# Kernel tuning notes

Hardware: AMD Instinct MI355X
Metric: run time of the kernel (lower is better)

## Reference

```python
import jax, jax.numpy as jnp
import numpy as np

T, N, D, H = 1024, 8, 1024, 16
DK = D // H
NEG_INF = jnp.finfo(jnp.float32).min


def setup_inputs() -> dict:
    key = jax.random.key(0)
    ks = jax.random.split(key, 4)
    x = jax.random.normal(ks[0], (T, N, D), dtype=jnp.float32)
    # xavier-uniform-like scale for in_proj, small scale for w_o
    w_in = jax.random.normal(ks[1], (3 * D, D), dtype=jnp.float32) * 0.02
    b_in = jnp.zeros((3 * D,), dtype=jnp.float32)
    w_o = jax.random.normal(ks[2], (D, D), dtype=jnp.float32) * 0.02
    b_o = jnp.zeros((D,), dtype=jnp.float32)
    # causal mask: True = masked (score set to -inf)
    attn_mask = jnp.triu(jnp.ones((T, T), dtype=bool), k=1)
    # key padding: pad tail positions per batch element; True = padded
    lens = jnp.array([1024, 1000, 900, 800, 1024, 950, 700, 600], dtype=jnp.int32)
    key_padding_mask = jnp.arange(T)[None, :] >= lens[:, None]  # [N, S]
    return {"x": x, "w_in": w_in, "b_in": b_in, "w_o": w_o, "b_o": b_o,
            "attn_mask": attn_mask, "key_padding_mask": key_padding_mask}


def reference(x, w_in, b_in, w_o, b_o, attn_mask, key_padding_mask):
    # self-attention path: fused QKV projection, then chunk(3, dim=-1)
    qkv = jnp.einsum('tnd,ed->tne', x, w_in) + b_in  # [T, N, 3D]
    q, k, v = jnp.split(qkv, 3, axis=-1)
    # [T, N, D] -> [T, N, H, DK]
    q = q.reshape(T, N, H, DK)
    k = k.reshape(T, N, H, DK)
    v = v.reshape(T, N, H, DK)
    scale = 1.0 / jnp.sqrt(jnp.float32(DK))
    # score: [N, H, T, S]
    score = jnp.einsum('tnhd,snhd->nhts', q, k) * scale
    score = jnp.where(attn_mask[None, None, :, :], NEG_INF, score)
    score = jnp.where(key_padding_mask[:, None, None, :], NEG_INF, score)
    p = jax.nn.softmax(score, axis=-1)  # dropout p=0.0 -> identity
    out = jnp.einsum('nhts,snhd->tnhd', p, v).reshape(T, N, D)
    out = jnp.einsum('tnd,ed->tne', out, w_o) + b_o
    return out
```

## Files before the change

kernel.cpp:

```cpp
#include <hip/hip_runtime.h>


#define T_SEQ 1024
#define NB 8
#define DMODEL 1024
#define NHEADS 16
#define DK 64

typedef __attribute__((ext_vector_type(8))) short bf16x8;
typedef __attribute__((ext_vector_type(8))) unsigned short u16x8;
typedef __attribute__((ext_vector_type(4))) float f32x4;

#define MFMA16(a, b, c) __builtin_amdgcn_mfma_f32_16x16x32_bf16((a), (b), (c), 0, 0, 0)
#define WAITVM(N) asm volatile("s_waitcnt vmcnt(" #N ")" ::: "memory")

__device__ __forceinline__ unsigned short f2bf(float f) {
  unsigned int u = __float_as_uint(f);
  unsigned int r = (u + 0x7FFFu + ((u >> 16) & 1u)) >> 16;
  return (unsigned short)r;
}

__device__ __forceinline__ float fexp2(float x) {
  float r;
  asm("v_exp_f32 %0, %1" : "=v"(r) : "v"(x));
  return r;
}

__device__ __forceinline__ unsigned cvtpk(float lo, float hi) {
  unsigned r;
  asm("v_cvt_pk_bf16_f32 %0, %1, %2" : "=v"(r) : "v"(lo), "v"(hi));
  return r;
}

__device__ __forceinline__ void gload16(const void* g, void* l) {
  __builtin_amdgcn_global_load_lds((const __attribute__((address_space(1))) void*)g,
                                   (__attribute__((address_space(3))) void*)l, 16, 0, 0);
}

#define XQ (T_SEQ * NB * DMODEL / 4)
#define WIQ (3 * DMODEL * DMODEL / 4)
#define WOQ (DMODEL * DMODEL / 4)

__global__ __launch_bounds__(256) void cvt_all(const float* __restrict__ x,
                                               const float* __restrict__ w_in,
                                               const float* __restrict__ w_o,
                                               unsigned short* __restrict__ xb,
                                               unsigned short* __restrict__ wib,
                                               unsigned short* __restrict__ wob,
                                               const void* __restrict__ kpm_raw,
                                               int* __restrict__ lens) {
  int i = blockIdx.x * blockDim.x + threadIdx.x;
  if (blockIdx.x == 0 && threadIdx.x < 64) {
    const int* ki = (const int*)kpm_raw;
    const unsigned char* kb = (const unsigned char*)kpm_raw;
    const int lane = threadIdx.x;
    int bad = 0;
    for (int j = lane; j < 2048; j += 64) {
      unsigned v = (unsigned)ki[j];
      bad |= (v != 0u && v != 1u && v != 0x3F800000u) ? 1 : 0;
    }
    for (int m = 1; m < 64; m <<= 1) bad |= __shfl_xor(bad, m);
    for (int n = 0; n < NB; ++n) {
      int cnt = 0;
      if (bad) {
        for (int s = lane; s < T_SEQ; s += 64) cnt += (kb[n * T_SEQ + s] == 0) ? 1 : 0;
      } else {
        for (int s = lane; s < T_SEQ; s += 64) cnt += (ki[n * T_SEQ + s] == 0) ? 1 : 0;
      }
      for (int m = 1; m < 64; m <<= 1) cnt += __shfl_xor(cnt, m);
      if (lane == 0) lens[n] = cnt;
    }
  }
  const float* src;
  unsigned short* dst;
  int j;
  if (i < XQ) {
    src = x; dst = xb; j = i;
  } else if (i < XQ + WIQ) {
    src = w_in; dst = wib; j = i - XQ;
  } else if (i < XQ + WIQ + WOQ) {
    src = w_o; dst = wob; j = i - XQ - WIQ;
  } else {
    return;
  }
  float4 v = reinterpret_cast<const float4*>(src)[j];
  uint2 o;
  o.x = (unsigned)f2bf(v.x) | ((unsigned)f2bf(v.y) << 16);
  o.y = (unsigned)f2bf(v.z) | ((unsigned)f2bf(v.w) << 16);
  reinterpret_cast<uint2*>(dst)[j] = o;
}

#define QSCALE 0.18033688f

template <int EPI>
__global__ __launch_bounds__(256) void gemm_bt_kernel(
    const unsigned short* __restrict__ A, const unsigned short* __restrict__ B,
    const float* __restrict__ bias, float* __restrict__ Cf,
    unsigned short* __restrict__ qb, unsigned short* __restrict__ kb,
    unsigned short* __restrict__ vtb, int M, int N, int K) {
  __shared__ unsigned short lds_all[64 * 136];
  unsigned short* lds_a = lds_all;
  unsigned short* lds_b = lds_all + 128 * 32;
  const int tid = threadIdx.x;
  const int brow = blockIdx.x * 128;
  const int bcol = blockIdx.y * 128;
  const int w = tid >> 6, lane = tid & 63;
  const int l15 = lane & 15, lg = lane >> 4;
  const int wr = (w >> 1) * 64, wc = (w & 1) * 64;

  f32x4 acc[4][4] = {};

  for (int k0 = 0; k0 < K; k0 += 32) {
#pragma unroll
    for (int i = 0; i < 2; ++i) {
      const int seg = i * 256 + tid;
      const int row = seg >> 2, slot = seg & 3;
      const int qq = (slot ^ ((row >> 1) & 3)) * 8;
      gload16(A + (size_t)(brow + row) * K + k0 + qq, lds_a + seg * 8);
      gload16(B + (size_t)(bcol + row) * K + k0 + qq, lds_b + seg * 8);
    }
    __syncthreads();
    bf16x8 af[4], bfr[4];
#pragma unroll
    for (int mi = 0; mi < 4; ++mi) {
      const int row = wr + mi * 16 + l15;
      af[mi] = *reinterpret_cast<const bf16x8*>(lds_a + row * 32 +
                                                ((lg ^ ((row >> 1) & 3)) << 3));
    }
#pragma unroll
    for (int ni = 0; ni < 4; ++ni) {
      const int row = wc + ni * 16 + l15;
      bfr[ni] = *reinterpret_cast<const bf16x8*>(lds_b + row * 32 +
                                                 ((lg ^ ((row >> 1) & 3)) << 3));
    }
#pragma unroll
    for (int mi = 0; mi < 4; ++mi)
#pragma unroll
      for (int ni = 0; ni < 4; ++ni)
        acc[mi][ni] = MFMA16(af[mi], bfr[ni], acc[mi][ni]);
    __syncthreads();
  }

  if (EPI == 0 && bcol >= 2 * DMODEL) {
    unsigned short* tl = lds_all;
    const int t0 = brow >> 3;
#pragma unroll
    for (int pass = 0; pass < 2; ++pass) {
      if ((w & 1) == pass) {
#pragma unroll
        for (int ni = 0; ni < 4; ++ni) {
          const int c = ni * 16 + l15;
          const float bv = bias[bcol + wc + ni * 16 + l15];
#pragma unroll
          for (int mi = 0; mi < 4; ++mi) {
#pragma unroll
            for (int r = 0; r < 4; ++r) {
              const int row = wr + mi * 16 + lg * 4 + r;
              const int tloc = row >> 3, nn = row & 7;
              tl[c * 136 + nn * 16 + tloc] = f2bf(acc[mi][ni][r] + bv);
            }
          }
        }
      }
      __syncthreads();
      const int hh = ((bcol + pass * 64) - 2 * DMODEL) >> 6;
#pragma unroll
      for (int it = 0; it < 2; ++it) {
        const int task = it * 256 + tid;
        const int c = task >> 3, nn = task & 7;
        const unsigned short* sp = &tl[c * 136 + nn * 16];
        const u16x8 lo = *reinterpret_cast<const u16x8*>(sp);
        const u16x8 hi = *reinterpret_cast<const u16x8*>(sp + 8);
        unsigned short* dst = vtb + (size_t)(nn * NHEADS + hh) * (T_SEQ * DK) +
                              (size_t)c * T_SEQ + t0;
        *reinterpret_cast<u16x8*>(dst) = lo;
        *reinterpret_cast<u16x8*>(dst + 8) = hi;
      }
      __syncthreads();
    }
    return;
  }

#pragma unroll
  for (int mi = 0; mi < 4; ++mi) {
#pragma unroll
    for (int ni = 0; ni < 4; ++ni) {
      const int col = bcol + wc + ni * 16 + l15;
      const float bv = bias[col];
      unsigned short* basep = nullptr;
      if (EPI == 0) basep = col < DMODEL ? qb : kb;
      const float scl = (EPI == 0 && col < DMODEL) ? QSCALE : 1.0f;
      const int c2 = col & (DMODEL - 1);
      const int hh = c2 >> 6, dk = c2 & 63;
#pragma unroll
      for (int r = 0; r < 4; ++r) {
        const int row = brow + wr + mi * 16 + lg * 4 + r;
        const float v = (acc[mi][ni][r] + bv) * scl;
        if (EPI == 1) {
          Cf[(size_t)row * N + col] = v;
        } else {
          const int t = row >> 3, n = row & 7;
          basep[(size_t)(n * NHEADS + hh) * (T_SEQ * DK) + t * DK + dk] = f2bf(v);
        }
      }
    }
  }
}

#define PLD 72

__device__ __forceinline__ void stage_kv(const unsigned short* kp_base,
                                         const unsigned short* vp_base, int s0,
                                         unsigned short* kl, unsigned short* vl, int tid) {
#pragma unroll
  for (int i = 0; i < 2; ++i) {
    const int seg = i * 256 + tid;
    const int r = seg >> 3, c8 = seg & 7;
    const int xc = (c8 ^ (r & 7)) * 8;
    gload16(kp_base + (((size_t)(s0 + r)) << 6) + xc, kl + seg * 8);
    gload16(vp_base + (size_t)r * T_SEQ + s0 + xc, vl + seg * 8);
  }
}

__global__ __launch_bounds__(256, 3) void attn_kernel(
    const unsigned short* __restrict__ qb, const unsigned short* __restrict__ kb,
    const unsigned short* __restrict__ vtb, const int* __restrict__ lens,
    unsigned short* __restrict__ attn_out) {
  __shared__ unsigned short k_lds[2][64 * 64];
  __shared__ unsigned short v_lds[2][64 * 64];
  __shared__ unsigned short p_lds[4 * 16 * PLD];
  const int bid = blockIdx.x;
  const int x = bid & 7;
  const int rem = bid >> 3;
  const int nh = (rem & 15) * 8 + x;
  const int pr = rem >> 4;
  const int n = nh >> 4;
  const int h = nh & 15;
  const int tid = threadIdx.x;
  const int w = tid >> 6, lane = tid & 63;
  const int l15 = lane & 15, lg = lane >> 4;
  const int len_n = lens[n];
  const int ltiles = (len_n + 63) >> 6;

  const unsigned short* kp_base = kb + (size_t)nh * (T_SEQ * DK);
  const unsigned short* vp_base = vtb + (size_t)nh * (T_SEQ * DK);
  const unsigned short* q_base = qb + (size_t)nh * (T_SEQ * DK);
  unsigned short* pw = p_lds + w * 16 * PLD;

  bf16x8 ones;
#pragma unroll
  for (int j = 0; j < 8; ++j) ones[j] = (short)0x3F80;

  const int qtA = pr, qtB = 15 - pr;
  int nA = qtA + 1, nB = qtB + 1;
  if (ltiles < nA) nA = ltiles;
  if (ltiles < nB) nB = ltiles;

  const unsigned short* qpA = q_base + (size_t)(qtA * 64 + w * 16 + l15) * DK;
  const unsigned short* qpB = q_base + (size_t)(qtB * 64 + w * 16 + l15) * DK;
  const bf16x8 qaA0 = *reinterpret_cast<const bf16x8*>(qpA + lg * 8);
  const bf16x8 qaA1 = *reinterpret_cast<const bf16x8*>(qpA + 32 + lg * 8);
  const bf16x8 qaB0 = *reinterpret_cast<const bf16x8*>(qpB + lg * 8);
  const bf16x8 qaB1 = *reinterpret_cast<const bf16x8*>(qpB + 32 + lg * 8);

  f32x4 oA[4] = {}, oB[4] = {};
  float lA[4] = {}, lB[4] = {};

  const int tbA = qtA * 64 + w * 16 + lg * 4;
  const int tbB = qtB * 64 + w * 16 + lg * 4;
  const int tlaneA = qtA * 64 + w * 16 + l15;
  const int tlaneB = qtB * 64 + w * 16 + l15;

  int cur = 0;
  stage_kv(kp_base, vp_base, 0, k_lds[0], v_lds[0], tid);

  for (int tile = 0; tile < nB; ++tile) {
    const int s0 = tile * 64;
    if (tile + 1 < nB) {
      stage_kv(kp_base, vp_base, s0 + 64, k_lds[cur ^ 1], v_lds[cur ^ 1], tid);
      WAITVM(4);
    } else {
      WAITVM(0);
    }
    __builtin_amdgcn_s_barrier();

    const bool actA = tile < nA;

    f32x4 sA[4] = {}, sB[4] = {};
    __builtin_amdgcn_s_setprio(1);
#pragma unroll
    for (int ct = 0; ct < 4; ++ct) {
      const int rl = ct * 16 + l15;
      const int c0 = lg ^ (rl & 7);
      const bf16x8 kf0 = *reinterpret_cast<const bf16x8*>(&k_lds[cur][rl * 64 + c0 * 8]);
      const bf16x8 kf1 = *reinterpret_cast<const bf16x8*>(&k_lds[cur][rl * 64 + (c0 ^ 4) * 8]);
      if (actA) {
        sA[ct] = MFMA16(kf0, qaA0, sA[ct]);
        sA[ct] = MFMA16(kf1, qaA1, sA[ct]);
      }
      sB[ct] = MFMA16(kf0, qaB0, sB[ct]);
      sB[ct] = MFMA16(kf1, qaB1, sB[ct]);
    }
    __builtin_amdgcn_s_setprio(0);
    bf16x8 vf[4][2];
#pragma unroll
    for (int ct = 0; ct < 4; ++ct) {
      const int rl = ct * 16 + l15;
      const int c0 = lg ^ (rl & 7);
      vf[ct][0] = *reinterpret_cast<const bf16x8*>(&v_lds[cur][rl * 64 + c0 * 8]);
      vf[ct][1] = *reinterpret_cast<const bf16x8*>(&v_lds[cur][rl * 64 + (c0 ^ 4) * 8]);
    }
    const int boundary = ((tile + 1) << 6) > len_n;

    if (actA) {
      if ((tile == qtA) | boundary) {
#pragma unroll
        for (int ct = 0; ct < 4; ++ct) {
          const int sb = s0 + ct * 16 + lg * 4;
#pragma unroll
          for (int r = 0; r < 4; ++r)
            if (sb + r > tlaneA || sb + r >= len_n) sA[ct][r] = -1e30f;
        }
      }
#pragma unroll
      for (int ct = 0; ct < 4; ++ct) {
        uint2 pk;
        pk.x = cvtpk(fexp2(sA[ct][0]), fexp2(sA[ct][1]));
        pk.y = cvtpk(fexp2(sA[ct][2]), fexp2(sA[ct][3]));
        *reinterpret_cast<uint2*>(pw + l15 * PLD + ct * 16 + lg * 4) = pk;
      }
      const bf16x8 pa0 = *reinterpret_cast<const bf16x8*>(pw + l15 * PLD + lg * 8);
      const bf16x8 pa1 = *reinterpret_cast<const bf16x8*>(pw + l15 * PLD + 32 + lg * 8);
      f32x4 lacc = {};
      __builtin_amdgcn_s_setprio(1);
      lacc = MFMA16(pa0, ones, lacc);
      lacc = MFMA16(pa1, ones, lacc);
#pragma unroll
      for (int ct = 0; ct < 4; ++ct) {
        oA[ct] = MFMA16(pa0, vf[ct][0], oA[ct]);
        oA[ct] = MFMA16(pa1, vf[ct][1], oA[ct]);
      }
      __builtin_amdgcn_s_setprio(0);
#pragma unroll
      for (int r = 0; r < 4; ++r) lA[r] += lacc[r];
    }

    {
      if ((tile == qtB) | boundary) {
#pragma unroll
        for (int ct = 0; ct < 4; ++ct) {
          const int sb = s0 + ct * 16 + lg * 4;
#pragma unroll
          for (int r = 0; r < 4; ++r)
            if (sb + r > tlaneB || sb + r >= len_n) sB[ct][r] = -1e30f;
        }
      }
#pragma unroll
      for (int ct = 0; ct < 4; ++ct) {
        uint2 pk;
        pk.x = cvtpk(fexp2(sB[ct][0]), fexp2(sB[ct][1]));
        pk.y = cvtpk(fexp2(sB[ct][2]), fexp2(sB[ct][3]));
        *reinterpret_cast<uint2*>(pw + l15 * PLD + ct * 16 + lg * 4) = pk;
      }
      const bf16x8 pa0 = *reinterpret_cast<const bf16x8*>(pw + l15 * PLD + lg * 8);
      const bf16x8 pa1 = *reinterpret_cast<const bf16x8*>(pw + l15 * PLD + 32 + lg * 8);
      f32x4 lacc = {};
      __builtin_amdgcn_s_setprio(1);
      lacc = MFMA16(pa0, ones, lacc);
      lacc = MFMA16(pa1, ones, lacc);
#pragma unroll
      for (int ct = 0; ct < 4; ++ct) {
        oB[ct] = MFMA16(pa0, vf[ct][0], oB[ct]);
        oB[ct] = MFMA16(pa1, vf[ct][1], oB[ct]);
      }
      __builtin_amdgcn_s_setprio(0);
#pragma unroll
      for (int r = 0; r < 4; ++r) lB[r] += lacc[r];
    }

    __builtin_amdgcn_s_barrier();
    cur ^= 1;
  }

#pragma unroll
  for (int r = 0; r < 4; ++r) { lA[r] = 1.0f / lA[r]; lB[r] = 1.0f / lB[r]; }
#pragma unroll
  for (int ct = 0; ct < 4; ++ct) {
    const int d = h * DK + ct * 16 + l15;
#pragma unroll
    for (int r = 0; r < 4; ++r) {
      attn_out[((size_t)(tbA + r) * NB + n) * DMODEL + d] = f2bf(oA[ct][r] * lA[r]);
      attn_out[((size_t)(tbB + r) * NB + n) * DMODEL + d] = f2bf(oB[ct][r] * lB[r]);
    }
  }
}

extern "C" void kernel_launch(void* const* d_in, const int* in_sizes, int n_in,
                              void* d_out, int out_size, void* d_ws, size_t ws_size,
                              hipStream_t stream) {
  const float* x = (const float*)d_in[0];
  const float* w_in = (const float*)d_in[1];
  const float* b_in = (const float*)d_in[2];
  const float* w_o = (const float*)d_in[3];
  const float* b_o = (const float*)d_in[4];
  const void* kpm = (const void*)d_in[6];
  float* out = (float*)d_out;

  char* ws = (char*)d_ws;
  unsigned short* x_bf = (unsigned short*)(ws + 0);
  unsigned short* win_bf = (unsigned short*)(ws + 16777216);
  unsigned short* wo_bf = (unsigned short*)(ws + 23068672);
  unsigned short* qb = (unsigned short*)(ws + 25165824);
  unsigned short* kb = (unsigned short*)(ws + 41943040);
  unsigned short* vtb = (unsigned short*)(ws + 58720256);
  unsigned short* attn_bf = (unsigned short*)(ws + 0);
  int* lens = (int*)(ws + 92274688);

  cvt_all<<<(XQ + WIQ + WOQ + 255) / 256, 256, 0, stream>>>(x, w_in, w_o, x_bf, win_bf, wo_bf,
                                                            kpm, lens);
  gemm_bt_kernel<0><<<dim3(64, 24), 256, 0, stream>>>(x_bf, win_bf, b_in, nullptr, qb, kb, vtb,
                                                      T_SEQ * NB, 3 * DMODEL, DMODEL);
  attn_kernel<<<NB * NHEADS * 8, 256, 0, stream>>>(qb, kb, vtb, lens, attn_bf);
  gemm_bt_kernel<1><<<dim3(64, 8), 256, 0, stream>>>(attn_bf, wo_bf, b_o, out, nullptr, nullptr,
                                                     nullptr, T_SEQ * NB, DMODEL, DMODEL);
}
```

Measured before the change: 169.6 us.

## Double-buffer LDS tiles in GEMM to overlap global loads with MFMA

Adds a two-stage LDS ping-pong buffer to the bf16 GEMM main loop. The next K-tile is prefetched with direct-to-LDS loads while the current tile runs through MFMA, and a partial vmcnt wait replaces the full __syncthreads drain. The aim is to hide global load latency. In exchange it doubles LDS use to 32KB, which may lower occupancy. It also relies on raw s_barrier and vmcnt counting being correct for LDS visibility, and the epilogue that reuses lds_all still needs adequate synchronization.

```diff
diff --git a/kernel.cpp b/kernel.cpp
--- a/kernel.cpp
+++ b/kernel.cpp
@@ -98,9 +98,7 @@
     const float* __restrict__ bias, float* __restrict__ Cf,
     unsigned short* __restrict__ qb, unsigned short* __restrict__ kb,
     unsigned short* __restrict__ vtb, int M, int N, int K) {
-  __shared__ unsigned short lds_all[64 * 136];
-  unsigned short* lds_a = lds_all;
-  unsigned short* lds_b = lds_all + 128 * 32;
+  __shared__ unsigned short lds_all[2 * 8192];
   const int tid = threadIdx.x;
   const int brow = blockIdx.x * 128;
   const int bcol = blockIdx.y * 128;
@@ -109,28 +107,46 @@
   const int wr = (w >> 1) * 64, wc = (w & 1) * 64;
 
   f32x4 acc[4][4] = {};
-
-  for (int k0 = 0; k0 < K; k0 += 32) {
+  const int KT = K >> 5;
+
+  auto stage = [&](int t, int buf) {
+    const int k0 = t << 5;
+    unsigned short* la = lds_all + buf * 8192;
+    unsigned short* lb = la + 4096;
 #pragma unroll
     for (int i = 0; i < 2; ++i) {
       const int seg = i * 256 + tid;
       const int row = seg >> 2, slot = seg & 3;
       const int qq = (slot ^ ((row >> 1) & 3)) * 8;
-      gload16(A + (size_t)(brow + row) * K + k0 + qq, lds_a + seg * 8);
-      gload16(B + (size_t)(bcol + row) * K + k0 + qq, lds_b + seg * 8);
-    }
-    __syncthreads();
+      gload16(A + (size_t)(brow + row) * K + k0 + qq, la + seg * 8);
+      gload16(B + (size_t)(bcol + row) * K + k0 + qq, lb + seg * 8);
+    }
+  };
+
+  stage(0, 0);
+  for (int t = 0; t < KT; ++t) {
+    const int cur = t & 1;
+    if (t + 1 < KT) {
+      stage(t + 1, cur ^ 1);
+      WAITVM(4);
+    } else {
+      WAITVM(0);
+    }
+    __builtin_amdgcn_s_barrier();
+
+    const unsigned short* la = lds_all + cur * 8192;
+    const unsigned short* lb = la + 4096;
     bf16x8 af[4], bfr[4];
 #pragma unroll
     for (int mi = 0; mi < 4; ++mi) {
       const int row = wr + mi * 16 + l15;
-      af[mi] = *reinterpret_cast<const bf16x8*>(lds_a + row * 32 +
+      af[mi] = *reinterpret_cast<const bf16x8*>(la + row * 32 +
                                                 ((lg ^ ((row >> 1) & 3)) << 3));
     }
 #pragma unroll
     for (int ni = 0; ni < 4; ++ni) {
       const int row = wc + ni * 16 + l15;
-      bfr[ni] = *reinterpret_cast<const bf16x8*>(lds_b + row * 32 +
+      bfr[ni] = *reinterpret_cast<const bf16x8*>(lb + row * 32 +
                                                  ((lg ^ ((row >> 1) & 3)) << 3));
     }
 #pragma unroll
@@ -138,7 +154,7 @@
 #pragma unroll
       for (int ni = 0; ni < 4; ++ni)
         acc[mi][ni] = MFMA16(af[mi], bfr[ni], acc[mi][ni]);
-    __syncthreads();
+    __builtin_amdgcn_s_barrier();
   }
 
   if (EPI == 0 && bcol >= 2 * DMODEL) {
```

Result: faster. 146.9 us (-13.4%).
